# Performance work log

Measured on AMD Instinct MI355X. Metric: run time of the kernel, lower is better.

The kernel has to match this reference:

```python
import jax, jax.numpy as jnp
import numpy as np

LN_EPS = 1e-5  # torch.nn.LayerNorm default


def setup_inputs() -> dict:
    key = jax.random.key(0)
    k1, k2, k3 = jax.random.split(key, 3)
    B, N, F, D = 8, 2048, 128, 128
    A_hat = jax.random.uniform(k1, (B, N, N), dtype=jnp.float32)
    X = jax.random.normal(k2, (B, N, F), dtype=jnp.float32)
    W = jax.random.normal(k3, (D, F), dtype=jnp.float32) * (1.0 / np.sqrt(F))
    b = jnp.zeros((D,), dtype=jnp.float32)
    gamma = jnp.ones((D,), dtype=jnp.float32)
    beta = jnp.zeros((D,), dtype=jnp.float32)
    return {"A_hat": A_hat, "X": X, "W": W, "b": b, "gamma": gamma, "beta": beta}


def reference(A_hat, X, W, b, gamma, beta):
    # batched aggregation: H[b] = A_hat[b] @ X[b]   (torch loop over batch, vectorized here)
    H = jnp.einsum('bnm,bmf->bnf', A_hat, X)
    # linear: torch nn.Linear stores W as [out, in]
    H = jnp.einsum('bnf,df->bnd', H, W) + b
    # LayerNorm over last dim, then ReLU (dropout p=0 -> identity)
    mu = jnp.mean(H, axis=-1, keepdims=True)
    var = jnp.mean((H - mu) ** 2, axis=-1, keepdims=True)
    Hn = (H - mu) * jax.lax.rsqrt(var + LN_EPS) * gamma + beta
    return jax.nn.relu(Hn)
```

## Files before the change

### kernel.cpp

```cpp
#include <hip/hip_runtime.h>
#include <stdint.h>

#define B_DIM 8
#define N_DIM 2048
#define F_DIM 128
#define D_DIM 128
#define LN_EPS 1e-5f

typedef __attribute__((ext_vector_type(8))) short short8;
typedef __attribute__((ext_vector_type(4))) float floatx4;

__device__ __forceinline__ ushort f2bf(float f) {
    union { float f; uint32_t u; } c;
    c.f = f;
    uint32_t u = c.u;
    return (ushort)((u + 0x7FFFu + ((u >> 16) & 1u)) >> 16);
}

__device__ __forceinline__ float bf2f(ushort u) {
    union { uint32_t u; float f; } c;
    c.u = ((uint32_t)u) << 16;
    return c.f;
}

__device__ __forceinline__ void load_lds16(const ushort* g, ushort* l) {
    __builtin_amdgcn_global_load_lds(
        (const __attribute__((address_space(1))) void*)g,
        (__attribute__((address_space(3))) void*)l,
        16, 0, 0);
}

__global__ __launch_bounds__(256) void k_transpose(const float* __restrict__ X,
                                                   ushort* __restrict__ Xt) {
    __shared__ ushort tile[64 * 65];
    const int t = threadIdx.x;
    const int b = blockIdx.z;
    const int k0 = blockIdx.x * 64;
    const int f0 = blockIdx.y * 64;

#pragma unroll
    for (int p = 0; p < 2; ++p) {
        int idx = p * 256 + t;
        int kk = idx >> 3;
        int ff = (idx & 7) * 8;
        const float* src = X + (((size_t)b * N_DIM) + k0 + kk) * F_DIM + f0 + ff;
        float4 v0 = *(const float4*)(src);
        float4 v1 = *(const float4*)(src + 4);
        ushort* d = tile + kk * 65 + ff;
        d[0] = f2bf(v0.x); d[1] = f2bf(v0.y); d[2] = f2bf(v0.z); d[3] = f2bf(v0.w);
        d[4] = f2bf(v1.x); d[5] = f2bf(v1.y); d[6] = f2bf(v1.z); d[7] = f2bf(v1.w);
    }
    __syncthreads();

    union U { uint4 v; ushort s[8]; };
#pragma unroll
    for (int p = 0; p < 2; ++p) {
        int idx = p * 256 + t;
        int f2 = idx >> 3;
        int kk2 = (idx & 7) * 8;
        U u;
#pragma unroll
        for (int j = 0; j < 8; ++j) u.s[j] = tile[(kk2 + j) * 65 + f2];
        *(uint4*)(Xt + (((size_t)b * F_DIM) + f0 + f2) * N_DIM + k0 + kk2) = u.v;
    }
}

#define BK 64
__global__ __launch_bounds__(256) void k_gemm(const float* __restrict__ A,
                                              const ushort* __restrict__ Xt,
                                              ushort* __restrict__ H) {
    __shared__ __align__(16) ushort As[32 * BK];
    __shared__ __align__(16) ushort Bs[128 * BK];
    const int t = threadIdx.x;
    const int lane = t & 63;
    const int w = t >> 6;
    const int q = lane >> 4;
    const int mr = lane & 15;
    const int bb = blockIdx.y;
    const int m0 = blockIdx.x * 32;

    const float* Ab = A + ((size_t)bb * N_DIM + m0) * N_DIM;
    const ushort* Xb = Xt + (size_t)bb * F_DIM * N_DIM;

    floatx4 acc[2][2];
#pragma unroll
    for (int i = 0; i < 2; ++i)
#pragma unroll
        for (int j = 0; j < 2; ++j) acc[i][j] = (floatx4){0.f, 0.f, 0.f, 0.f};

    const int am = t >> 3;
    const int akc = t & 7;
    const float* a_src = Ab + (size_t)am * N_DIM + akc * 8;
    ushort* a_dst = As + ((am * 8) + (akc ^ (am & 7))) * 8;

    const ushort* b_src[4];
    ushort* b_dst[4];
#pragma unroll
    for (int p = 0; p < 4; ++p) {
        int c = p * 256 + t;
        int n = c >> 3;
        int kl = (c & 7) ^ (n & 7);
        b_src[p] = Xb + (size_t)n * N_DIM + kl * 8;
        b_dst[p] = Bs + c * 8;
    }

    for (int k0 = 0; k0 < N_DIM; k0 += BK) {
#pragma unroll
        for (int p = 0; p < 4; ++p) load_lds16(b_src[p] + k0, b_dst[p]);

        float4 v0 = *(const float4*)(a_src + k0);
        float4 v1 = *(const float4*)(a_src + k0 + 4);
        short8 ap;
        ap[0] = (short)f2bf(v0.x); ap[1] = (short)f2bf(v0.y);
        ap[2] = (short)f2bf(v0.z); ap[3] = (short)f2bf(v0.w);
        ap[4] = (short)f2bf(v1.x); ap[5] = (short)f2bf(v1.y);
        ap[6] = (short)f2bf(v1.z); ap[7] = (short)f2bf(v1.w);
        *(short8*)a_dst = ap;
        __syncthreads();

#pragma unroll
        for (int ks = 0; ks < 2; ++ks) {
            short8 af[2], bf[2];
#pragma unroll
            for (int i = 0; i < 2; ++i) {
                int m = mr + i * 16;
                int chunk = m * 8 + ((ks * 4 + q) ^ (m & 7));
                af[i] = *(const short8*)(As + chunk * 8);
            }
#pragma unroll
            for (int j = 0; j < 2; ++j) {
                int n = w * 32 + j * 16 + mr;
                int chunk = n * 8 + ((ks * 4 + q) ^ (n & 7));
                bf[j] = *(const short8*)(Bs + chunk * 8);
            }
#pragma unroll
            for (int i = 0; i < 2; ++i)
#pragma unroll
                for (int j = 0; j < 2; ++j)
                    acc[i][j] = __builtin_amdgcn_mfma_f32_16x16x32_bf16(
                        af[i], bf[j], acc[i][j], 0, 0, 0);
        }
        __syncthreads();
    }

#pragma unroll
    for (int i = 0; i < 2; ++i)
#pragma unroll
        for (int j = 0; j < 2; ++j)
#pragma unroll
            for (int r = 0; r < 4; ++r) {
                int grow = m0 + i * 16 + q * 4 + r;
                int gcol = w * 32 + j * 16 + mr;
                H[((size_t)bb * N_DIM + grow) * F_DIM + gcol] = f2bf(acc[i][j][r]);
            }
}

__global__ __launch_bounds__(256) void k_linear_ln(const ushort* __restrict__ H,
                                                   const float* __restrict__ W,
                                                   const float* __restrict__ bias,
                                                   const float* __restrict__ gamma,
                                                   const float* __restrict__ beta,
                                                   float* __restrict__ out) {
    __shared__ __align__(16) ushort Ws[128 * 136];
    __shared__ __align__(16) ushort Hs[32 * 136];
    __shared__ __align__(16) float Yt[32][132];

    const int t = threadIdx.x;
    const int lane = t & 63;
    const int w = t >> 6;
    const int q = lane >> 4;
    const int mr = lane & 15;
    const size_t r0 = (size_t)blockIdx.x * 32;

#pragma unroll
    for (int p = 0; p < 8; ++p) {
        int c = p * 256 + t;
        int d = c >> 4;
        int ff = (c & 15) * 8;
        const float* src = W + d * 128 + ff;
        float4 v0 = *(const float4*)(src);
        float4 v1 = *(const float4*)(src + 4);
        short8 pk;
        pk[0] = (short)f2bf(v0.x); pk[1] = (short)f2bf(v0.y);
        pk[2] = (short)f2bf(v0.z); pk[3] = (short)f2bf(v0.w);
        pk[4] = (short)f2bf(v1.x); pk[5] = (short)f2bf(v1.y);
        pk[6] = (short)f2bf(v1.z); pk[7] = (short)f2bf(v1.w);
        *(short8*)(Ws + d * 136 + ff) = pk;
    }
#pragma unroll
    for (int p = 0; p < 2; ++p) {
        int c = p * 256 + t;
        int m = c >> 4;
        int ff = (c & 15) * 8;
        uint4 v = *(const uint4*)(H + (r0 + m) * 128 + ff);
        *(uint4*)(Hs + m * 136 + ff) = v;
    }
    __syncthreads();

    floatx4 acc[2][2];
#pragma unroll
    for (int i = 0; i < 2; ++i)
#pragma unroll
        for (int j = 0; j < 2; ++j) acc[i][j] = (floatx4){0.f, 0.f, 0.f, 0.f};

#pragma unroll
    for (int ks = 0; ks < 4; ++ks) {
        short8 a0 = *(const short8*)(Hs + mr * 136 + ks * 32 + q * 8);
        short8 a1 = *(const short8*)(Hs + (mr + 16) * 136 + ks * 32 + q * 8);
        short8 b0 = *(const short8*)(Ws + (w * 32 + mr) * 136 + ks * 32 + q * 8);
        short8 b1 = *(const short8*)(Ws + (w * 32 + 16 + mr) * 136 + ks * 32 + q * 8);
        acc[0][0] = __builtin_amdgcn_mfma_f32_16x16x32_bf16(a0, b0, acc[0][0], 0, 0, 0);
        acc[0][1] = __builtin_amdgcn_mfma_f32_16x16x32_bf16(a0, b1, acc[0][1], 0, 0, 0);
        acc[1][0] = __builtin_amdgcn_mfma_f32_16x16x32_bf16(a1, b0, acc[1][0], 0, 0, 0);
        acc[1][1] = __builtin_amdgcn_mfma_f32_16x16x32_bf16(a1, b1, acc[1][1], 0, 0, 0);
    }

    float bv[2] = { bias[w * 32 + mr], bias[w * 32 + 16 + mr] };
#pragma unroll
    for (int i = 0; i < 2; ++i)
#pragma unroll
        for (int j = 0; j < 2; ++j)
#pragma unroll
            for (int r = 0; r < 4; ++r)
                Yt[i * 16 + q * 4 + r][w * 32 + j * 16 + mr] = acc[i][j][r] + bv[j];
    __syncthreads();

    const int row = t >> 3;
    const int seg = t & 7;
    float v[16];
    float s = 0.f, s2 = 0.f;
#pragma unroll
    for (int u = 0; u < 16; ++u) {
        v[u] = Yt[row][seg * 16 + u];
        s += v[u];
        s2 += v[u] * v[u];
    }
    s  += __shfl_xor(s, 1);  s2 += __shfl_xor(s2, 1);
    s  += __shfl_xor(s, 2);  s2 += __shfl_xor(s2, 2);
    s  += __shfl_xor(s, 4);  s2 += __shfl_xor(s2, 4);
    float mu = s * (1.0f / 128.0f);
    float var = s2 * (1.0f / 128.0f) - mu * mu;
    float rs = rsqrtf(var + LN_EPS);

    float4 ov[4];
    float* ovf = (float*)ov;
#pragma unroll
    for (int u = 0; u < 16; ++u) {
        int d = seg * 16 + u;
        float y = (v[u] - mu) * rs * gamma[d] + beta[d];
        ovf[u] = fmaxf(y, 0.0f);
    }
    float4* dst = (float4*)(out + (r0 + row) * 128 + seg * 16);
    dst[0] = ov[0]; dst[1] = ov[1]; dst[2] = ov[2]; dst[3] = ov[3];
}

extern "C" void kernel_launch(void* const* d_in, const int* in_sizes, int n_in,
                              void* d_out, int out_size, void* d_ws, size_t ws_size,
                              hipStream_t stream) {
    const float* A     = (const float*)d_in[0];
    const float* X     = (const float*)d_in[1];
    const float* W     = (const float*)d_in[2];
    const float* bias  = (const float*)d_in[3];
    const float* gamma = (const float*)d_in[4];
    const float* beta  = (const float*)d_in[5];
    float* out = (float*)d_out;

    ushort* Xt = (ushort*)d_ws;
    ushort* H  = Xt + (size_t)B_DIM * F_DIM * N_DIM;

    k_transpose<<<dim3(32, 2, 8), 256, 0, stream>>>(X, Xt);
    k_gemm<<<dim3(64, 8), 256, 0, stream>>>(A, Xt, H);
    k_linear_ln<<<dim3(512), 256, 0, stream>>>(H, W, bias, gamma, beta, out);
}
```

Measured before the change: 223.5 us.

## Fuse aggregation GEMM with linear+LayerNorm and stream operands directly from global

Merges the A@X GEMM and the linear+LayerNorm+ReLU kernels into one 512-thread kernel per 32-row tile, keeping H in LDS instead of writing and rereading it through global memory. The main loop drops LDS staging and barriers: each wave loads A and Xt fragments straight from global into registers, prefetching one k-step ahead. W is converted per wave from global. Risks include less data reuse, since each wave reloads the A rows on its own, and uncoalesced global fragment loads. Rounding changes to round-half-up.

```diff
diff --git a/kernel.cpp b/kernel.cpp
--- a/kernel.cpp
+++ b/kernel.cpp
@@ -4,7 +4,6 @@
 #define B_DIM 8
 #define N_DIM 2048
 #define F_DIM 128
-#define D_DIM 128
 #define LN_EPS 1e-5f
 
 typedef __attribute__((ext_vector_type(8))) short short8;
@@ -17,17 +16,25 @@
     return (ushort)((u + 0x7FFFu + ((u >> 16) & 1u)) >> 16);
 }
 
-__device__ __forceinline__ float bf2f(ushort u) {
-    union { uint32_t u; float f; } c;
-    c.u = ((uint32_t)u) << 16;
-    return c.f;
-}
-
-__device__ __forceinline__ void load_lds16(const ushort* g, ushort* l) {
-    __builtin_amdgcn_global_load_lds(
-        (const __attribute__((address_space(1))) void*)g,
-        (__attribute__((address_space(3))) void*)l,
-        16, 0, 0);
+__device__ __forceinline__ uint32_t pk2bf(float a, float b) {
+    union { float f; uint32_t u; } x, y;
+    x.f = a; y.f = b;
+    return ((x.u + 0x8000u) >> 16) | ((y.u + 0x8000u) & 0xFFFF0000u);
+}
+
+__device__ __forceinline__ short8 pack8(float4 lo, float4 hi) {
+    union { uint32_t u[4]; short8 s; } r;
+    r.u[0] = pk2bf(lo.x, lo.y);
+    r.u[1] = pk2bf(lo.z, lo.w);
+    r.u[2] = pk2bf(hi.x, hi.y);
+    r.u[3] = pk2bf(hi.z, hi.w);
+    return r.s;
+}
+
+__device__ __forceinline__ short8 asw(uint4 v) {
+    union { uint4 v; short8 s; } r;
+    r.v = v;
+    return r.s;
 }
 
 __global__ __launch_bounds__(256) void k_transpose(const float* __restrict__ X,
@@ -65,193 +72,128 @@
     }
 }
 
-#define BK 64
-__global__ __launch_bounds__(256) void k_gemm(const float* __restrict__ A,
-                                              const ushort* __restrict__ Xt,
-                                              ushort* __restrict__ H) {
-    __shared__ __align__(16) ushort As[32 * BK];
-    __shared__ __align__(16) ushort Bs[128 * BK];
+__global__ __launch_bounds__(512) void k_fused(const float* __restrict__ A,
+                                               const ushort* __restrict__ Xt,
+                                               const float* __restrict__ W,
+                                               const float* __restrict__ bias,
+                                               const float* __restrict__ gamma,
+                                               const float* __restrict__ beta,
+                                               float* __restrict__ out) {
+    __shared__ __align__(16) ushort Ht[32 * 136];
+    __shared__ float Pt[32][132];
+
     const int t = threadIdx.x;
     const int lane = t & 63;
     const int w = t >> 6;
     const int q = lane >> 4;
     const int mr = lane & 15;
-    const int bb = blockIdx.y;
-    const int m0 = blockIdx.x * 32;
-
-    const float* Ab = A + ((size_t)bb * N_DIM + m0) * N_DIM;
-    const ushort* Xb = Xt + (size_t)bb * F_DIM * N_DIM;
-
-    floatx4 acc[2][2];
-#pragma unroll
-    for (int i = 0; i < 2; ++i)
-#pragma unroll
-        for (int j = 0; j < 2; ++j) acc[i][j] = (floatx4){0.f, 0.f, 0.f, 0.f};
-
-    const int am = t >> 3;
-    const int akc = t & 7;
-    const float* a_src = Ab + (size_t)am * N_DIM + akc * 8;
-    ushort* a_dst = As + ((am * 8) + (akc ^ (am & 7))) * 8;
-
-    const ushort* b_src[4];
-    ushort* b_dst[4];
-#pragma unroll
-    for (int p = 0; p < 4; ++p) {
-        int c = p * 256 + t;
-        int n = c >> 3;
-        int kl = (c & 7) ^ (n & 7);
-        b_src[p] = Xb + (size_t)n * N_DIM + kl * 8;
-        b_dst[p] = Bs + c * 8;
-    }
-
-    for (int k0 = 0; k0 < N_DIM; k0 += BK) {
-#pragma unroll
-        for (int p = 0; p < 4; ++p) load_lds16(b_src[p] + k0, b_dst[p]);
-
-        float4 v0 = *(const float4*)(a_src + k0);
-        float4 v1 = *(const float4*)(a_src + k0 + 4);
-        short8 ap;
-        ap[0] = (short)f2bf(v0.x); ap[1] = (short)f2bf(v0.y);
-        ap[2] = (short)f2bf(v0.z); ap[3] = (short)f2bf(v0.w);
-        ap[4] = (short)f2bf(v1.x); ap[5] = (short)f2bf(v1.y);
-        ap[6] = (short)f2bf(v1.z); ap[7] = (short)f2bf(v1.w);
-        *(short8*)a_dst = ap;
-        __syncthreads();
-
-#pragma unroll
-        for (int ks = 0; ks < 2; ++ks) {
-            short8 af[2], bf[2];
-#pragma unroll
-            for (int i = 0; i < 2; ++i) {
-                int m = mr + i * 16;
-                int chunk = m * 8 + ((ks * 4 + q) ^ (m & 7));
-                af[i] = *(const short8*)(As + chunk * 8);
-            }
-#pragma unroll
-            for (int j = 0; j < 2; ++j) {
-                int n = w * 32 + j * 16 + mr;
-                int chunk = n * 8 + ((ks * 4 + q) ^ (n & 7));
-                bf[j] = *(const short8*)(Bs + chunk * 8);
-            }
-#pragma unroll
-            for (int i = 0; i < 2; ++i)
-#pragma unroll
-                for (int j = 0; j < 2; ++j)
-                    acc[i][j] = __builtin_amdgcn_mfma_f32_16x16x32_bf16(
-                        af[i], bf[j], acc[i][j], 0, 0, 0);
+
+    const int bid = blockIdx.x;
+    const int bb = bid & 7;
+    const int m0 = (bid >> 3) * 32;
+
+    const float* A0 = A + ((size_t)bb * N_DIM + m0 + mr) * N_DIM + q * 8;
+    const float* A1 = A0 + (size_t)16 * N_DIM;
+    const ushort* Bp = Xt + ((size_t)bb * F_DIM + w * 16 + mr) * N_DIM + q * 8;
+
+    floatx4 acc0 = {0.f, 0.f, 0.f, 0.f};
+    floatx4 acc1 = {0.f, 0.f, 0.f, 0.f};
+
+    float4 a0l = ((const float4*)A0)[0];
+    float4 a0h = ((const float4*)A0)[1];
+    float4 a1l = ((const float4*)A1)[0];
+    float4 a1h = ((const float4*)A1)[1];
+    uint4 bv = *(const uint4*)Bp;
+
+#pragma unroll 3
+    for (int ks = 0; ks < 63; ++ks) {
+        const float* pA0 = A0 + (ks + 1) * 32;
+        const float* pA1 = A1 + (ks + 1) * 32;
+        const ushort* pB = Bp + (ks + 1) * 32;
+        float4 n0l = ((const float4*)pA0)[0];
+        float4 n0h = ((const float4*)pA0)[1];
+        float4 n1l = ((const float4*)pA1)[0];
+        float4 n1h = ((const float4*)pA1)[1];
+        uint4 nb = *(const uint4*)pB;
+
+        short8 bf = asw(bv);
+        acc0 = __builtin_amdgcn_mfma_f32_16x16x32_bf16(pack8(a0l, a0h), bf, acc0, 0, 0, 0);
+        acc1 = __builtin_amdgcn_mfma_f32_16x16x32_bf16(pack8(a1l, a1h), bf, acc1, 0, 0, 0);
+
+        a0l = n0l; a0h = n0h; a1l = n1l; a1h = n1h; bv = nb;
+    }
+    {
+        short8 bf = asw(bv);
+        acc0 = __builtin_amdgcn_mfma_f32_16x16x32_bf16(pack8(a0l, a0h), bf, acc0, 0, 0, 0);
+        acc1 = __builtin_amdgcn_mfma_f32_16x16x32_bf16(pack8(a1l, a1h), bf, acc1, 0, 0, 0);
+    }
+
+    {
+        int col = w * 16 + mr;
+#pragma unroll
+        for (int r = 0; r < 4; ++r) {
+            union { float f; uint32_t u; } c0, c1;
+            c0.f = acc0[r]; c1.f = acc1[r];
+            Ht[(q * 4 + r) * 136 + col] = (ushort)((c0.u + 0x8000u + ((c0.u >> 16) & 1u) - 1u + 0x7FFFu - 0x7FFEu) >> 16);
+            Ht[(16 + q * 4 + r) * 136 + col] = (ushort)((c1.u + 0x8000u) >> 16);
         }
-        __syncthreads();
-    }
-
-#pragma unroll
-    for (int i = 0; i < 2; ++i)
-#pragma unroll
-        for (int j = 0; j < 2; ++j)
-#pragma unroll
-            for (int r = 0; r < 4; ++r) {
-                int grow = m0 + i * 16 + q * 4 + r;
-                int gcol = w * 32 + j * 16 + mr;
-                H[((size_t)bb * N_DIM + grow) * F_DIM + gcol] = f2bf(acc[i][j][r]);
-            }
-}
-
-__global__ __launch_bounds__(256) void k_linear_ln(const ushort* __restrict__ H,
-                                                   const float* __restrict__ W,
-                                                   const float* __restrict__ bias,
-                                                   const float* __restrict__ gamma,
-                                                   const float* __restrict__ beta,
-                                                   float* __restrict__ out) {
-    __shared__ __align__(16) ushort Ws[128 * 136];
-    __shared__ __align__(16) ushort Hs[32 * 136];
-    __shared__ __align__(16) float Yt[32][132];
-
-    const int t = threadIdx.x;
-    const int lane = t & 63;
-    const int w = t >> 6;
-    const int q = lane >> 4;
-    const int mr = lane & 15;
-    const size_t r0 = (size_t)blockIdx.x * 32;
-
-#pragma unroll
-    for (int p = 0; p < 8; ++p) {
-        int c = p * 256 + t;
-        int d = c >> 4;
-        int ff = (c & 15) * 8;
-        const float* src = W + d * 128 + ff;
-        float4 v0 = *(const float4*)(src);
-        float4 v1 = *(const float4*)(src + 4);
-        short8 pk;
-        pk[0] = (short)f2bf(v0.x); pk[1] = (short)f2bf(v0.y);
-        pk[2] = (short)f2bf(v0.z); pk[3] = (short)f2bf(v0.w);
-        pk[4] = (short)f2bf(v1.x); pk[5] = (short)f2bf(v1.y);
-        pk[6] = (short)f2bf(v1.z); pk[7] = (short)f2bf(v1.w);
-        *(short8*)(Ws + d * 136 + ff) = pk;
-    }
-#pragma unroll
-    for (int p = 0; p < 2; ++p) {
-        int c = p * 256 + t;
-        int m = c >> 4;
-        int ff = (c & 15) * 8;
-        uint4 v = *(const uint4*)(H + (r0 + m) * 128 + ff);
-        *(uint4*)(Hs + m * 136 + ff) = v;
     }
     __syncthreads();
 
-    floatx4 acc[2][2];
-#pragma unroll
-    for (int i = 0; i < 2; ++i)
-#pragma unroll
-        for (int j = 0; j < 2; ++j) acc[i][j] = (floatx4){0.f, 0.f, 0.f, 0.f};
-
+    floatx4 p0 = {0.f, 0.f, 0.f, 0.f};
+    floatx4 p1 = {0.f, 0.f, 0.f, 0.f};
+    const float* Wp = W + (w * 16 + mr) * F_DIM + q * 8;
 #pragma unroll
     for (int ks = 0; ks < 4; ++ks) {
-        short8 a0 = *(const short8*)(Hs + mr * 136 + ks * 32 + q * 8);
-        short8 a1 = *(const short8*)(Hs + (mr + 16) * 136 + ks * 32 + q * 8);
-        short8 b0 = *(const short8*)(Ws + (w * 32 + mr) * 136 + ks * 32 + q * 8);
-        short8 b1 = *(const short8*)(Ws + (w * 32 + 16 + mr) * 136 + ks * 32 + q * 8);
-        acc[0][0] = __builtin_amdgcn_mfma_f32_16x16x32_bf16(a0, b0, acc[0][0], 0, 0, 0);
-        acc[0][1] = __builtin_amdgcn_mfma_f32_16x16x32_bf16(a0, b1, acc[0][1], 0, 0, 0);
-        acc[1][0] = __builtin_amdgcn_mfma_f32_16x16x32_bf16(a1, b0, acc[1][0], 0, 0, 0);
-        acc[1][1] = __builtin_amdgcn_mfma_f32_16x16x32_bf16(a1, b1, acc[1][1], 0, 0, 0);
-    }
-
-    float bv[2] = { bias[w * 32 + mr], bias[w * 32 + 16 + mr] };
-#pragma unroll
-    for (int i = 0; i < 2; ++i)
-#pragma unroll
-        for (int j = 0; j < 2; ++j)
-#pragma unroll
-            for (int r = 0; r < 4; ++r)
-                Yt[i * 16 + q * 4 + r][w * 32 + j * 16 + mr] = acc[i][j][r] + bv[j];
+        short8 ha0 = *(const short8*)(Ht + mr * 136 + ks * 32 + q * 8);
+        short8 ha1 = *(const short8*)(Ht + (mr + 16) * 136 + ks * 32 + q * 8);
+        float4 wl = ((const float4*)(Wp + ks * 32))[0];
+        float4 wh = ((const float4*)(Wp + ks * 32))[1];
+        short8 wb = pack8(wl, wh);
+        p0 = __builtin_amdgcn_mfma_f32_16x16x32_bf16(ha0, wb, p0, 0, 0, 0);
+        p1 = __builtin_amdgcn_mfma_f32_16x16x32_bf16(ha1, wb, p1, 0, 0, 0);
+    }
+
+    {
+        int col = w * 16 + mr;
+        float bcol = bias[col];
+#pragma unroll
+        for (int r = 0; r < 4; ++r) {
+            Pt[q * 4 + r][col] = p0[r] + bcol;
+            Pt[16 + q * 4 + r][col] = p1[r] + bcol;
+        }
+    }
     __syncthreads();
 
-    const int row = t >> 3;
-    const int seg = t & 7;
-    float v[16];
+    const int row = t >> 4;
+    const int seg = t & 15;
+    float v[8];
     float s = 0.f, s2 = 0.f;
 #pragma unroll
-    for (int u = 0; u < 16; ++u) {
-        v[u] = Yt[row][seg * 16 + u];
+    for (int u = 0; u < 8; ++u) {
+        v[u] = Pt[row][seg * 8 + u];
         s += v[u];
         s2 += v[u] * v[u];
     }
-    s  += __shfl_xor(s, 1);  s2 += __shfl_xor(s2, 1);
-    s  += __shfl_xor(s, 2);  s2 += __shfl_xor(s2, 2);
-    s  += __shfl_xor(s, 4);  s2 += __shfl_xor(s2, 4);
+    s += __shfl_xor(s, 1);  s2 += __shfl_xor(s2, 1);
+    s += __shfl_xor(s, 2);  s2 += __shfl_xor(s2, 2);
+    s += __shfl_xor(s, 4);  s2 += __shfl_xor(s2, 4);
+    s += __shfl_xor(s, 8);  s2 += __shfl_xor(s2, 8);
     float mu = s * (1.0f / 128.0f);
     float var = s2 * (1.0f / 128.0f) - mu * mu;
     float rs = rsqrtf(var + LN_EPS);
 
-    float4 ov[4];
-    float* ovf = (float*)ov;
-#pragma unroll
-    for (int u = 0; u < 16; ++u) {
-        int d = seg * 16 + u;
+    float4 o[2];
+    float* of = (float*)o;
+#pragma unroll
+    for (int u = 0; u < 8; ++u) {
+        int d = seg * 8 + u;
         float y = (v[u] - mu) * rs * gamma[d] + beta[d];
-        ovf[u] = fmaxf(y, 0.0f);
-    }
-    float4* dst = (float4*)(out + (r0 + row) * 128 + seg * 16);
-    dst[0] = ov[0]; dst[1] = ov[1]; dst[2] = ov[2]; dst[3] = ov[3];
+        of[u] = fmaxf(y, 0.0f);
+    }
+    float4* dst = (float4*)(out + ((size_t)bb * N_DIM + m0 + row) * F_DIM + seg * 8);
+    dst[0] = o[0];
+    dst[1] = o[1];
 }
 
 extern "C" void kernel_launch(void* const* d_in, const int* in_sizes, int n_in,
@@ -266,9 +208,7 @@
     float* out = (float*)d_out;
 
     ushort* Xt = (ushort*)d_ws;
-    ushort* H  = Xt + (size_t)B_DIM * F_DIM * N_DIM;
 
     k_transpose<<<dim3(32, 2, 8), 256, 0, stream>>>(X, Xt);
-    k_gemm<<<dim3(64, 8), 256, 0, stream>>>(A, Xt, H);
-    k_linear_ln<<<dim3(512), 256, 0, stream>>>(H, W, bias, gamma, beta, out);
-}
+    k_fused<<<dim3(512), 512, 0, stream>>>(A, Xt, W, bias, gamma, beta, out);
+}
```

New measurement: 312.1 us. +39.7%, slower.
